# Performance work log

Measured on AMD Instinct MI355X. Metric: run time of the kernel, lower is better.

The kernel has to match this reference:

```python
import jax, jax.numpy as jnp
import numpy as np

N_NODES = 100000
N_EDGES = 3200000
D_IN, D_HID, D_OUT = 256, 256, 256
B, V, C = 64, 50, 64
DEC_H1, DEC_H2, N_CLS = 512, 256, 1000
NEG_INF = -1e9


def setup_inputs() -> dict:
    key = jax.random.key(0)
    ks = jax.random.split(key, 20)
    s = lambda d: 1.0 / np.sqrt(d)
    return {
        'edge_index': jax.random.randint(ks[0], (2, N_EDGES), 0, N_NODES, dtype=jnp.int64 if jax.config.jax_enable_x64 else jnp.int32),
        'edge_weight': jax.random.uniform(ks[1], (N_EDGES,), dtype=jnp.float32),
        'codes_x': jax.random.randint(ks[2], (B, V, C), 0, N_NODES, dtype=jnp.int64 if jax.config.jax_enable_x64 else jnp.int32),
        'node_emb': jax.random.normal(ks[3], (N_NODES, D_IN), jnp.float32) * 0.02,
        'W1': jax.random.normal(ks[4], (D_IN, D_HID), jnp.float32) * s(D_IN),
        'b1': jnp.zeros((D_HID,), jnp.float32),
        'W2': jax.random.normal(ks[5], (D_HID, D_OUT), jnp.float32) * s(D_HID),
        'b2': jnp.zeros((D_OUT,), jnp.float32),
        'Wv': jax.random.normal(ks[6], (D_OUT, D_OUT), jnp.float32) * s(D_OUT),
        'uv': jax.random.normal(ks[7], (D_OUT,), jnp.float32) * s(D_OUT),
        'Wp': jax.random.normal(ks[8], (D_OUT, D_OUT), jnp.float32) * s(D_OUT),
        'up': jax.random.normal(ks[9], (D_OUT,), jnp.float32) * s(D_OUT),
        'Wd1': jax.random.normal(ks[10], (D_OUT, DEC_H1), jnp.float32) * s(D_OUT),
        'bd1': jnp.zeros((DEC_H1,), jnp.float32),
        'Wd2': jax.random.normal(ks[11], (DEC_H1, DEC_H2), jnp.float32) * s(DEC_H1),
        'bd2': jnp.zeros((DEC_H2,), jnp.float32),
        'Wd3': jax.random.normal(ks[12], (DEC_H2, N_CLS), jnp.float32) * s(DEC_H2),
        'bd3': jnp.zeros((N_CLS,), jnp.float32),
    }


def reference(edge_index, edge_weight, codes_x, node_emb, W1, b1, W2, b2,
              Wv, uv, Wp, up, Wd1, bd1, Wd2, bd2, Wd3, bd3):
    n = node_emb.shape[0]
    src, dst = edge_index[0], edge_index[1]

    def agg(x):  # weighted message passing: out_i = sum_{e: dst=i} w_e * x[src_e]
        return jax.ops.segment_sum(x[src] * edge_weight[:, None], dst, num_segments=n)

    # 2-layer weighted GCN over the code ontology graph (dropout in eval mode)
    h = jax.nn.relu(agg(node_emb) @ W1 + b1)          # [N, D_hid]
    emb = agg(h) @ W2 + b2                             # [N, D_out]

    # Ragged per-visit code attention, vectorized with masks (code id 0 = padding)
    code_mask = codes_x > 0                            # [B, V, C]
    ce = emb[codes_x]                                  # [B, V, C, D]
    ev = jnp.tanh(jnp.einsum('bvcd,de->bvce', ce, Wv)) @ uv   # [B, V, C]
    av = jax.nn.softmax(jnp.where(code_mask, ev, NEG_INF), axis=-1)
    vemb = jnp.einsum('bvc,bvcd->bvd', av, ce)         # [B, V, D]
    visit_mask = code_mask.any(-1)                     # [B, V]
    vemb = jnp.where(visit_mask[..., None], vemb, 0.0)

    # Per-patient visit attention over valid visits only
    ep = jnp.tanh(vemb @ Wp) @ up                      # [B, V]
    ap = jax.nn.softmax(jnp.where(visit_mask, ep, NEG_INF), axis=-1)
    pemb = jnp.einsum('bv,bvd->bd', ap, vemb)          # [B, D]
    pemb = jnp.where(visit_mask.any(-1)[:, None], pemb, 0.0)  # empty patient -> zeros

    # Decoder MLP classifier (train_type='direct')
    h1 = jax.nn.relu(pemb @ Wd1 + bd1)
    h2 = jax.nn.relu(h1 @ Wd2 + bd2)
    return h2 @ Wd3 + bd3                              # [B, n_classes]
```

## Files before the change

### kernel.cpp

```cpp
#include <hip/hip_runtime.h>
#include <hip/hip_bf16.h>
#include <math.h>


#define D 256
#define BPAT 64
#define VIS 50
#define CODES 64
#define NEG_INF -1e9f
#define MPAD 100096
#define BINB 32
#define NBIN 3125
#define SORTCAP 1536

typedef unsigned short ushort_t;
typedef short short8 __attribute__((ext_vector_type(8)));
typedef float f32x4 __attribute__((ext_vector_type(4)));

__device__ __forceinline__ float blo(unsigned u) { return __uint_as_float(u << 16); }
__device__ __forceinline__ float bhi(unsigned u) { return __uint_as_float(u & 0xffff0000u); }
__device__ __forceinline__ float bf2f(ushort_t u) { return __uint_as_float((unsigned)u << 16); }
__device__ __forceinline__ ushort_t f2bfu(float f) {
    __hip_bfloat16 h = __float2bfloat16(f);
    return *reinterpret_cast<ushort_t*>(&h);
}
__device__ __forceinline__ unsigned pack2(float a, float b) {
    return (unsigned)f2bfu(a) | ((unsigned)f2bfu(b) << 16);
}
__device__ __forceinline__ float fast_tanh(float x) {
    return 1.f - 2.f / (__expf(2.f * x) + 1.f);
}

__global__ __launch_bounds__(512) void count_transpose_kernel(
    const int* __restrict__ ei, int* __restrict__ bincount, int ne,
    const float* __restrict__ Wa, const float* __restrict__ Wb,
    const float* __restrict__ Wc, const float* __restrict__ Wd,
    ushort_t* __restrict__ Ta, ushort_t* __restrict__ Tb,
    ushort_t* __restrict__ Tc, ushort_t* __restrict__ Td) {
    __shared__ int h[NBIN];
    __shared__ float tt[2][32][33];
    if (blockIdx.x < 256) {
        for (int i = threadIdx.x; i < NBIN; i += 512) h[i] = 0;
        __syncthreads();
        const int stride = 256 * 512;
        for (int e = blockIdx.x * 512 + threadIdx.x; e < ne; e += stride)
            atomicAdd(&h[ei[(size_t)ne + e] >> 5], 1);
        __syncthreads();
        for (int i = threadIdx.x; i < NBIN; i += 512) {
            int c = h[i];
            if (c) atomicAdd(&bincount[i], c);
        }
    } else {
        int tile = (blockIdx.x - 256) * 2 + (threadIdx.x >> 8);
        int which = tile >> 6, rem = tile & 63;
        int bx = (rem & 7) << 5, by = (rem >> 3) << 5;
        const float* W = (which == 0) ? Wa : (which == 1) ? Wb
                        : (which == 2) ? Wc : Wd;
        ushort_t* Wt = (which == 0) ? Ta : (which == 1) ? Tb
                      : (which == 2) ? Tc : Td;
        int hf = threadIdx.x >> 8;
        int ltid = threadIdx.x & 255;
        int lx = ltid & 31, ly = ltid >> 5;
        #pragma unroll
        for (int i = 0; i < 32; i += 8)
            tt[hf][ly + i][lx] = W[(size_t)(by + ly + i) * 256 + bx + lx];
        __syncthreads();
        #pragma unroll
        for (int i = 0; i < 32; i += 8)
            Wt[(size_t)(bx + ly + i) * 256 + by + lx] = f2bfu(tt[hf][lx][ly + i]);
    }
}

__global__ __launch_bounds__(64) void bin_scan_kernel(
    const int* __restrict__ bincount, int* __restrict__ binstart,
    int* __restrict__ bincursor, int* __restrict__ rp, int ne, int nn) {
    __shared__ int carry;
    int lane = threadIdx.x;
    if (lane == 0) carry = 0;
    __syncthreads();
    for (int base = 0; base < NBIN; base += 64) {
        int i = base + lane;
        int v = (i < NBIN) ? bincount[i] : 0;
        int x = v;
        #pragma unroll
        for (int d = 1; d < 64; d <<= 1) {
            int y = __shfl_up(x, (unsigned)d, 64);
            if (lane >= d) x += y;
        }
        int c = carry;
        if (i < NBIN) { int ex = c + x - v; binstart[i] = ex; bincursor[i] = ex; }
        __syncthreads();
        if (lane == 63) carry = c + x;
        __syncthreads();
    }
    if (lane == 0) { binstart[NBIN] = ne; rp[nn] = ne; }
}

__global__ __launch_bounds__(512) void part_gemm_kernel(
    const int* __restrict__ ei, const float* __restrict__ ew,
    int* __restrict__ bincursor, uint2* __restrict__ ptmp, int ne,
    const float* __restrict__ Af, const ushort_t* __restrict__ Wt,
    ushort_t* __restrict__ out, int nvalid) {
    __shared__ int h[NBIN];
    __shared__ int base_[NBIN];
    __shared__ __align__(16) ushort_t As[128 * 32];
    __shared__ __align__(16) ushort_t Bs[256 * 32];
    const int tid = threadIdx.x;
    if (blockIdx.x < 256) {
        for (int i = tid; i < NBIN; i += 512) h[i] = 0;
        __syncthreads();
        const int stride = 256 * 512;
        for (int e = blockIdx.x * 512 + tid; e < ne; e += stride)
            atomicAdd(&h[ei[(size_t)ne + e] >> 5], 1);
        __syncthreads();
        for (int i = tid; i < NBIN; i += 512) {
            int c = h[i];
            base_[i] = c ? atomicAdd(&bincursor[i], c) : 0;
            h[i] = 0;
        }
        __syncthreads();
        for (int e = blockIdx.x * 512 + tid; e < ne; e += stride) {
            int dd = ei[(size_t)ne + e];
            int ss = ei[e];
            float w = ew[e];
            int bin = dd >> 5;
            int r = atomicAdd(&h[bin], 1);
            ptmp[base_[bin] + r] =
                make_uint2((unsigned)ss | ((unsigned)(dd & 31) << 17),
                           __float_as_uint(w));
        }
        return;
    }
    const int gbid = blockIdx.x - 256;
    const int lane = tid & 63;
    const int wv = tid >> 6;
    const int wr = wv >> 2, wc = wv & 3;
    const size_t brow = (size_t)gbid * 128;

    const int ra = tid >> 2, ca = tid & 3;
    const int rb1 = ra + 128;
    const int csa = ca ^ ((ra >> 1) & 3);
    const int arow = (int)brow + ra;
    const bool aval = arow < nvalid;
    const float* gAf = Af + (size_t)arow * 256 + ca * 8;
    const ushort_t* gB0 = Wt + (size_t)ra  * 256 + ca * 8;
    const ushort_t* gB1 = Wt + (size_t)rb1 * 256 + ca * 8;
    ushort_t* lA  = As + ra * 32 + csa * 8;
    ushort_t* lB0 = Bs + ra * 32 + csa * 8;
    ushort_t* lB1 = Bs + rb1 * 32 + csa * 8;

    const int g = lane >> 4, rl = lane & 15;
    int aoff[4], boff[4];
    #pragma unroll
    for (int m = 0; m < 4; ++m) {
        int row = wr * 64 + m * 16 + rl;
        aoff[m] = row * 32 + (g ^ ((row >> 1) & 3)) * 8;
    }
    #pragma unroll
    for (int n = 0; n < 4; ++n) {
        int row = wc * 64 + n * 16 + rl;
        boff[n] = row * 32 + (g ^ ((row >> 1) & 3)) * 8;
    }

    f32x4 acc[4][4] = {};
    float4 pa0 = make_float4(0.f, 0.f, 0.f, 0.f), pa1 = pa0;
    if (aval) { pa0 = *(const float4*)gAf; pa1 = *(const float4*)(gAf + 4); }
    uint4 vb0 = *(const uint4*)gB0;
    uint4 vb1 = *(const uint4*)gB1;

    for (int ks = 0; ks < 8; ++ks) {
        uint4 va;
        va.x = pack2(pa0.x, pa0.y); va.y = pack2(pa0.z, pa0.w);
        va.z = pack2(pa1.x, pa1.y); va.w = pack2(pa1.z, pa1.w);
        *(uint4*)lA = va; *(uint4*)lB0 = vb0; *(uint4*)lB1 = vb1;
        __syncthreads();
        if (ks < 7) {
            int k0 = (ks + 1) * 32;
            if (aval) {
                pa0 = *(const float4*)(gAf + k0);
                pa1 = *(const float4*)(gAf + k0 + 4);
            }
            vb0 = *(const uint4*)(gB0 + k0);
            vb1 = *(const uint4*)(gB1 + k0);
        }
        short8 af[4], bfv[4];
        #pragma unroll
        for (int m = 0; m < 4; ++m) af[m] = *(const short8*)(As + aoff[m]);
        #pragma unroll
        for (int n = 0; n < 4; ++n) bfv[n] = *(const short8*)(Bs + boff[n]);
        #pragma unroll
        for (int m = 0; m < 4; ++m)
            #pragma unroll
            for (int n = 0; n < 4; ++n)
                acc[m][n] = __builtin_amdgcn_mfma_f32_16x16x32_bf16(
                    af[m], bfv[n], acc[m][n], 0, 0, 0);
        __syncthreads();
    }

    #pragma unroll
    for (int m = 0; m < 4; ++m) {
        #pragma unroll
        for (int r = 0; r < 4; ++r) {
            size_t row = brow + wr * 64 + m * 16 + g * 4 + r;
            #pragma unroll
            for (int n = 0; n < 4; ++n) {
                int col = wc * 64 + n * 16 + rl;
                out[row * 256 + col] = f2bfu(acc[m][n][r]);
            }
        }
    }
}

__global__ __launch_bounds__(256) void binsort_kernel(
    const uint2* __restrict__ ptmp, const int* __restrict__ binstart,
    uint2* __restrict__ epair, int* __restrict__ rp) {
    int b = blockIdx.x;
    int tid = threadIdx.x;
    int beg = binstart[b], end = binstart[b + 1];
    int nE = end - beg;
    __shared__ uint2 sbuf[SORTCAP];
    __shared__ int cnt[BINB];
    __shared__ int cur[BINB];
    if (tid < BINB) cnt[tid] = 0;
    __syncthreads();
    if (nE <= SORTCAP) {
        for (int i = tid; i < nE; i += 256) {
            uint2 p = ptmp[beg + i];
            sbuf[i] = p;
            atomicAdd(&cnt[(p.x >> 17) & 31], 1);
        }
        __syncthreads();
        if (tid < BINB) {
            int v = cnt[tid];
            int x = v;
            #pragma unroll
            for (int d = 1; d < BINB; d <<= 1) {
                int y = __shfl_up(x, (unsigned)d, BINB);
                if (tid >= d) x += y;
            }
            int start = beg + x - v;
            cur[tid] = start;
            rp[b * BINB + tid] = start;
        }
        __syncthreads();
        for (int i = tid; i < nE; i += 256) {
            uint2 p = sbuf[i];
            int dl = (p.x >> 17) & 31;
            int pos = atomicAdd(&cur[dl], 1);
            epair[pos] = make_uint2(p.x & 0x1FFFF, p.y);
        }
    } else {
        for (int i = beg + tid; i < end; i += 256)
            atomicAdd(&cnt[(ptmp[i].x >> 17) & 31], 1);
        __syncthreads();
        if (tid < BINB) {
            int v = cnt[tid];
            int x = v;
            #pragma unroll
            for (int d = 1; d < BINB; d <<= 1) {
                int y = __shfl_up(x, (unsigned)d, BINB);
                if (tid >= d) x += y;
            }
            int start = beg + x - v;
            cur[tid] = start;
            rp[b * BINB + tid] = start;
        }
        __syncthreads();
        for (int i = beg + tid; i < end; i += 256) {
            uint2 p = ptmp[i];
            int dl = (p.x >> 17) & 31;
            int pos = atomicAdd(&cur[dl], 1);
            epair[pos] = make_uint2(p.x & 0x1FFFF, p.y);
        }
    }
}

__device__ __forceinline__ void acc8(float* a, uint4 v, float w) {
    a[0] += w * blo(v.x); a[1] += w * bhi(v.x);
    a[2] += w * blo(v.y); a[3] += w * bhi(v.y);
    a[4] += w * blo(v.z); a[5] += w * bhi(v.z);
    a[6] += w * blo(v.w); a[7] += w * bhi(v.w);
}

template<int ACT>
__global__ __launch_bounds__(256) void agg_bf16_kernel(
    const ushort_t* __restrict__ x, const int* __restrict__ rp,
    const uint2* __restrict__ ep, const float* __restrict__ bias,
    ushort_t* __restrict__ out, int n) {
    int wv = (int)(((size_t)blockIdx.x * blockDim.x + threadIdx.x) >> 6);
    int lane = threadIdx.x & 63;
    if (wv >= n) return;
    int half = lane >> 5;
    int l32 = lane & 31;
    int beg = rp[wv], end = rp[wv + 1];
    float a[8] = {};
    int e = beg;
    for (; e + 16 <= end; e += 16) {
        uint2 p0 = ep[e + half];
        uint2 p1 = ep[e + 2 + half];
        uint2 p2 = ep[e + 4 + half];
        uint2 p3 = ep[e + 6 + half];
        uint2 p4 = ep[e + 8 + half];
        uint2 p5 = ep[e + 10 + half];
        uint2 p6 = ep[e + 12 + half];
        uint2 p7 = ep[e + 14 + half];
        uint4 v0 = ((const uint4*)(x + (size_t)p0.x * D))[l32];
        uint4 v1 = ((const uint4*)(x + (size_t)p1.x * D))[l32];
        uint4 v2 = ((const uint4*)(x + (size_t)p2.x * D))[l32];
        uint4 v3 = ((const uint4*)(x + (size_t)p3.x * D))[l32];
        uint4 v4 = ((const uint4*)(x + (size_t)p4.x * D))[l32];
        uint4 v5 = ((const uint4*)(x + (size_t)p5.x * D))[l32];
        uint4 v6 = ((const uint4*)(x + (size_t)p6.x * D))[l32];
        uint4 v7 = ((const uint4*)(x + (size_t)p7.x * D))[l32];
        acc8(a, v0, __uint_as_float(p0.y));
        acc8(a, v1, __uint_as_float(p1.y));
        acc8(a, v2, __uint_as_float(p2.y));
        acc8(a, v3, __uint_as_float(p3.y));
        acc8(a, v4, __uint_as_float(p4.y));
        acc8(a, v5, __uint_as_float(p5.y));
        acc8(a, v6, __uint_as_float(p6.y));
        acc8(a, v7, __uint_as_float(p7.y));
    }
    for (; e + 4 <= end; e += 4) {
        uint2 p0 = ep[e + half];
        uint2 p1 = ep[e + 2 + half];
        uint4 v0 = ((const uint4*)(x + (size_t)p0.x * D))[l32];
        uint4 v1 = ((const uint4*)(x + (size_t)p1.x * D))[l32];
        acc8(a, v0, __uint_as_float(p0.y));
        acc8(a, v1, __uint_as_float(p1.y));
    }
    for (; e + 2 <= end; e += 2) {
        uint2 p0 = ep[e + half];
        uint4 v0 = ((const uint4*)(x + (size_t)p0.x * D))[l32];
        acc8(a, v0, __uint_as_float(p0.y));
    }
    if (e < end) {
        uint2 p0 = ep[e];
        uint4 v0 = ((const uint4*)(x + (size_t)p0.x * D))[l32];
        acc8(a, v0, half ? 0.f : __uint_as_float(p0.y));
    }
    #pragma unroll
    for (int j = 0; j < 8; ++j) a[j] += __shfl_xor(a[j], 32, 64);
    if (half == 0) {
        float4 b0 = ((const float4*)bias)[l32 * 2];
        float4 b1 = ((const float4*)bias)[l32 * 2 + 1];
        a[0] += b0.x; a[1] += b0.y; a[2] += b0.z; a[3] += b0.w;
        a[4] += b1.x; a[5] += b1.y; a[6] += b1.z; a[7] += b1.w;
        if (ACT == 1) {
            #pragma unroll
            for (int j = 0; j < 8; ++j) a[j] = fmaxf(a[j], 0.f);
        }
        uint4 o;
        o.x = pack2(a[0], a[1]); o.y = pack2(a[2], a[3]);
        o.z = pack2(a[4], a[5]); o.w = pack2(a[6], a[7]);
        ((uint4*)(out + (size_t)wv * D))[l32] = o;
    }
}

template<int MODE>
__global__ __launch_bounds__(512) void mfma_gemm_kernel(
    const ushort_t* __restrict__ A, const ushort_t* __restrict__ Wt,
    const float* __restrict__ bias, ushort_t* __restrict__ out,
    const float* __restrict__ u, float* __restrict__ tout, int mvalid) {
    __shared__ __align__(16) ushort_t As[128 * 32];
    __shared__ __align__(16) ushort_t Bs[256 * 32];
    __shared__ float s_t[128];
    const int tid = threadIdx.x;
    const int lane = tid & 63;
    const int wv = tid >> 6;
    const int wr = wv >> 2, wc = wv & 3;
    const size_t brow = (size_t)blockIdx.x * 128;

    const int ra = tid >> 2, ca = tid & 3;
    const int rb1 = ra + 128;
    const int csa = ca ^ ((ra >> 1) & 3);
    const ushort_t* gA  = A  + (brow + ra) * 256 + ca * 8;
    const ushort_t* gB0 = Wt + (size_t)ra  * 256 + ca * 8;
    const ushort_t* gB1 = Wt + (size_t)rb1 * 256 + ca * 8;
    ushort_t* lA  = As + ra * 32 + csa * 8;
    ushort_t* lB0 = Bs + ra * 32 + csa * 8;
    ushort_t* lB1 = Bs + rb1 * 32 + csa * 8;

    const int g = lane >> 4, rl = lane & 15;
    int aoff[4], boff[4];
    #pragma unroll
    for (int m = 0; m < 4; ++m) {
        int row = wr * 64 + m * 16 + rl;
        aoff[m] = row * 32 + (g ^ ((row >> 1) & 3)) * 8;
    }
    #pragma unroll
    for (int n = 0; n < 4; ++n) {
        int row = wc * 64 + n * 16 + rl;
        boff[n] = row * 32 + (g ^ ((row >> 1) & 3)) * 8;
    }

    if (MODE == 2 && tid < 128) s_t[tid] = 0.f;

    f32x4 acc[4][4] = {};
    uint4 va  = *(const uint4*)gA;
    uint4 vb0 = *(const uint4*)gB0;
    uint4 vb1 = *(const uint4*)gB1;

    for (int ks = 0; ks < 8; ++ks) {
        *(uint4*)lA = va; *(uint4*)lB0 = vb0; *(uint4*)lB1 = vb1;
        __syncthreads();
        if (ks < 7) {
            int k0 = (ks + 1) * 32;
            va  = *(const uint4*)(gA + k0);
            vb0 = *(const uint4*)(gB0 + k0);
            vb1 = *(const uint4*)(gB1 + k0);
        }
        short8 af[4], bfv[4];
        #pragma unroll
        for (int m = 0; m < 4; ++m) af[m] = *(const short8*)(As + aoff[m]);
        #pragma unroll
        for (int n = 0; n < 4; ++n) bfv[n] = *(const short8*)(Bs + boff[n]);
        #pragma unroll
        for (int m = 0; m < 4; ++m)
            #pragma unroll
            for (int n = 0; n < 4; ++n)
                acc[m][n] = __builtin_amdgcn_mfma_f32_16x16x32_bf16(
                    af[m], bfv[n], acc[m][n], 0, 0, 0);
        __syncthreads();
    }

    if (MODE == 2) {
        float uvv[4];
        #pragma unroll
        for (int n = 0; n < 4; ++n) uvv[n] = u[wc * 64 + n * 16 + rl];
        #pragma unroll
        for (int m = 0; m < 4; ++m) {
            #pragma unroll
            for (int r = 0; r < 4; ++r) {
                float v = 0.f;
                #pragma unroll
                for (int n = 0; n < 4; ++n) v += fast_tanh(acc[m][n][r]) * uvv[n];
                v += __shfl_xor(v, 1, 64);
                v += __shfl_xor(v, 2, 64);
                v += __shfl_xor(v, 4, 64);
                v += __shfl_xor(v, 8, 64);
                if (rl == 0) atomicAdd(&s_t[wr * 64 + m * 16 + g * 4 + r], v);
            }
        }
        __syncthreads();
        if (tid < 128 && brow + tid < (size_t)mvalid) tout[brow + tid] = s_t[tid];
    } else {
        #pragma unroll
        for (int m = 0; m < 4; ++m) {
            #pragma unroll
            for (int r = 0; r < 4; ++r) {
                size_t row = brow + wr * 64 + m * 16 + g * 4 + r;
                #pragma unroll
                for (int n = 0; n < 4; ++n) {
                    int col = wc * 64 + n * 16 + rl;
                    float v = acc[m][n][r] + (bias ? bias[col] : 0.f);
                    out[row * 256 + col] = f2bfu(v);
                }
            }
        }
    }
}

__global__ __launch_bounds__(256) void code_attn_kernel(
    const int* __restrict__ codes, const float* __restrict__ t,
    const ushort_t* __restrict__ emb, ushort_t* __restrict__ vembB,
    int* __restrict__ vmask) {
    int bv = blockIdx.x;
    int tid = threadIdx.x;
    __shared__ int s_codes[CODES];
    __shared__ float s_av[CODES];
    __shared__ int s_valid;
    if (tid < 64) {
        int c = codes[(size_t)bv * CODES + tid];
        s_codes[tid] = c;
        float e = (c > 0) ? t[c] : NEG_INF;
        float m = e;
        #pragma unroll
        for (int d = 32; d; d >>= 1) m = fmaxf(m, __shfl_xor(m, d, 64));
        float ex = expf(e - m);
        float s = ex;
        #pragma unroll
        for (int d = 32; d; d >>= 1) s += __shfl_xor(s, d, 64);
        s_av[tid] = ex / s;
        if (tid == 0) s_valid = (m > -1e8f) ? 1 : 0;
    }
    __syncthreads();
    float acc = 0.f;
    #pragma unroll 8
    for (int c = 0; c < CODES; ++c)
        acc += s_av[c] * bf2f(emb[(size_t)s_codes[c] * D + tid]);
    int valid = s_valid;
    vembB[(size_t)bv * D + tid] = f2bfu(valid ? acc : 0.f);
    if (tid == 0) vmask[bv] = valid;
}

__global__ __launch_bounds__(512) void patient_dec_kernel(
    const ushort_t* __restrict__ vembB, const float* __restrict__ epr,
    const int* __restrict__ vmask,
    const float* __restrict__ Wd1, const float* __restrict__ bd1,
    const float* __restrict__ Wd2, const float* __restrict__ bd2,
    const float* __restrict__ Wd3, const float* __restrict__ bd3,
    float* __restrict__ outp) {
    int b = blockIdx.x;
    int tid = threadIdx.x;
    __shared__ float s_ap[VIS];
    __shared__ float s_x[256];
    __shared__ float s_h1[512];
    __shared__ float s_h2[256];
    __shared__ int s_any;

    if (tid < 64) {
        float e = -3e38f;
        if (tid < VIS) e = vmask[b * VIS + tid] ? epr[b * VIS + tid] : NEG_INF;
        float m = e;
        #pragma unroll
        for (int d = 32; d; d >>= 1) m = fmaxf(m, __shfl_xor(m, d, 64));
        float ex = (tid < VIS) ? expf(e - m) : 0.f;
        float s = ex;
        #pragma unroll
        for (int d = 32; d; d >>= 1) s += __shfl_xor(s, d, 64);
        if (tid < VIS) s_ap[tid] = ex / s;
        if (tid == 0) s_any = (m > -1e8f) ? 1 : 0;
    }
    __syncthreads();
    if (tid < 256) {
        float acc = 0.f;
        for (int v = 0; v < VIS; ++v)
            acc += s_ap[v] * bf2f(vembB[((size_t)b * VIS + v) * D + tid]);
        s_x[tid] = s_any ? acc : 0.f;
    }
    __syncthreads();
    {
        float acc = bd1[tid];
        #pragma unroll 8
        for (int k = 0; k < 256; ++k)
            acc = fmaf(s_x[k], Wd1[(size_t)k * 512 + tid], acc);
        s_h1[tid] = fmaxf(acc, 0.f);
    }
    __syncthreads();
    if (tid < 256) {
        float acc = bd2[tid];
        #pragma unroll 8
        for (int k = 0; k < 512; ++k)
            acc = fmaf(s_h1[k], Wd2[(size_t)k * 256 + tid], acc);
        s_h2[tid] = fmaxf(acc, 0.f);
    }
    __syncthreads();
    for (int j = tid; j < 1000; j += 512) {
        float acc = bd3[j];
        #pragma unroll 8
        for (int k = 0; k < 256; ++k)
            acc = fmaf(s_h2[k], Wd3[(size_t)k * 1000 + j], acc);
        outp[(size_t)b * 1000 + j] = acc;
    }
}

extern "C" void kernel_launch(void* const* d_in, const int* in_sizes, int n_in,
                              void* d_out, int out_size, void* d_ws, size_t ws_size,
                              hipStream_t stream) {
    const int* edge_index    = (const int*)d_in[0];
    const float* edge_weight = (const float*)d_in[1];
    const int* codes         = (const int*)d_in[2];
    const float* node_emb    = (const float*)d_in[3];
    const float* W1 = (const float*)d_in[4];
    const float* b1 = (const float*)d_in[5];
    const float* W2 = (const float*)d_in[6];
    const float* b2 = (const float*)d_in[7];
    const float* Wv = (const float*)d_in[8];
    const float* uv = (const float*)d_in[9];
    const float* Wp = (const float*)d_in[10];
    const float* up = (const float*)d_in[11];
    const float* Wd1 = (const float*)d_in[12];
    const float* bd1 = (const float*)d_in[13];
    const float* Wd2 = (const float*)d_in[14];
    const float* bd2 = (const float*)d_in[15];
    const float* Wd3 = (const float*)d_in[16];
    const float* bd3 = (const float*)d_in[17];

    const int NE = in_sizes[1];
    const int NN = in_sizes[3] / D;

    char* ws = (char*)d_ws;
    size_t off = 0;
    auto alloc = [&](size_t bytes) -> void* {
        void* p = ws + off;
        off += (bytes + 255) & ~(size_t)255;
        return p;
    };
    ushort_t* zbuf = (ushort_t*)alloc((size_t)MPAD * D * 2);
    ushort_t* hbuf = (ushort_t*)alloc((size_t)MPAD * D * 2);
    ushort_t* embB = (ushort_t*)alloc((size_t)MPAD * D * 2);
    uint2* ptmp   = (uint2*)alloc((size_t)NE * 8);
    uint2* epair  = (uint2*)alloc((size_t)NE * 8);
    int* bincount = (int*)alloc((size_t)NBIN * 4);
    int* binstart = (int*)alloc((size_t)(NBIN + 1) * 4);
    int* bincursor= (int*)alloc((size_t)NBIN * 4);
    int* rp       = (int*)alloc((size_t)(NN + 1) * 4);
    ushort_t* W1t = (ushort_t*)alloc(256 * 256 * 2);
    ushort_t* W2t = (ushort_t*)alloc(256 * 256 * 2);
    ushort_t* Wvt = (ushort_t*)alloc(256 * 256 * 2);
    ushort_t* Wpt = (ushort_t*)alloc(256 * 256 * 2);
    float* tbuf  = (float*)alloc((size_t)NN * 4);
    ushort_t* vembB = (ushort_t*)alloc((size_t)BPAT * VIS * D * 2);
    int*   vmask = (int*)  alloc((size_t)BPAT * VIS * 4);
    float* epr   = (float*)alloc((size_t)BPAT * VIS * 4);
    (void)ws_size; (void)n_in; (void)out_size;

    const int ab = NN / 4;

    hipMemsetAsync(bincount, 0, (size_t)NBIN * 4, stream);
    count_transpose_kernel<<<256 + 128, 512, 0, stream>>>(
        edge_index, bincount, NE, W1, W2, Wv, Wp, W1t, W2t, Wvt, Wpt);
    bin_scan_kernel<<<1, 64, 0, stream>>>(bincount, binstart, bincursor, rp, NE, NN);
    part_gemm_kernel<<<256 + MPAD / 128, 512, 0, stream>>>(
        edge_index, edge_weight, bincursor, ptmp, NE,
        node_emb, W1t, zbuf, NN);
    binsort_kernel<<<NBIN, 256, 0, stream>>>(ptmp, binstart, epair, rp);

    agg_bf16_kernel<1><<<ab, 256, 0, stream>>>(zbuf, rp, epair, b1, hbuf, NN);

    mfma_gemm_kernel<1><<<MPAD / 128, 512, 0, stream>>>(
        hbuf, W2t, nullptr, zbuf, nullptr, nullptr, 0);
    agg_bf16_kernel<0><<<ab, 256, 0, stream>>>(zbuf, rp, epair, b2, embB, NN);

    mfma_gemm_kernel<2><<<MPAD / 128, 512, 0, stream>>>(
        embB, Wvt, nullptr, nullptr, uv, tbuf, NN);

    code_attn_kernel<<<BPAT * VIS, 256, 0, stream>>>(codes, tbuf, embB, vembB, vmask);

    mfma_gemm_kernel<2><<<BPAT * VIS / 128, 512, 0, stream>>>(
        vembB, Wpt, nullptr, nullptr, up, epr, BPAT * VIS);

    patient_dec_kernel<<<BPAT, 512, 0, stream>>>(
        vembB, epr, vmask, Wd1, bd1, Wd2, bd2, Wd3, bd3, (float*)d_out);
}
```

Baseline: 794.6 us.

## Split edge aggregation into two feature-half passes to shrink gather working set

```diff
diff --git a/kernel.cpp b/kernel.cpp
--- a/kernel.cpp
+++ b/kernel.cpp
@@ -275,15 +275,13 @@
     }
 }
 
-__device__ __forceinline__ void acc8(float* a, uint4 v, float w) {
+__device__ __forceinline__ void acc4(float* a, uint2 v, float w) {
     a[0] += w * blo(v.x); a[1] += w * bhi(v.x);
     a[2] += w * blo(v.y); a[3] += w * bhi(v.y);
-    a[4] += w * blo(v.z); a[5] += w * bhi(v.z);
-    a[6] += w * blo(v.w); a[7] += w * bhi(v.w);
-}
-
-template<int ACT>
-__global__ __launch_bounds__(256) void agg_bf16_kernel(
+}
+
+template<int ACT, int PASS>
+__global__ __launch_bounds__(256) void agg_half_kernel(
     const ushort_t* __restrict__ x, const int* __restrict__ rp,
     const uint2* __restrict__ ep, const float* __restrict__ bias,
     ushort_t* __restrict__ out, int n) {
@@ -293,7 +291,8 @@
     int half = lane >> 5;
     int l32 = lane & 31;
     int beg = rp[wv], end = rp[wv + 1];
-    float a[8] = {};
+    const ushort_t* xh = x + PASS * 128;
+    float a[4] = {};
     int e = beg;
     for (; e + 16 <= end; e += 16) {
         uint2 p0 = ep[e + half];
@@ -304,56 +303,53 @@
         uint2 p5 = ep[e + 10 + half];
         uint2 p6 = ep[e + 12 + half];
         uint2 p7 = ep[e + 14 + half];
-        uint4 v0 = ((const uint4*)(x + (size_t)p0.x * D))[l32];
-        uint4 v1 = ((const uint4*)(x + (size_t)p1.x * D))[l32];
-        uint4 v2 = ((const uint4*)(x + (size_t)p2.x * D))[l32];
-        uint4 v3 = ((const uint4*)(x + (size_t)p3.x * D))[l32];
-        uint4 v4 = ((const uint4*)(x + (size_t)p4.x * D))[l32];
-        uint4 v5 = ((const uint4*)(x + (size_t)p5.x * D))[l32];
-        uint4 v6 = ((const uint4*)(x + (size_t)p6.x * D))[l32];
-        uint4 v7 = ((const uint4*)(x + (size_t)p7.x * D))[l32];
-        acc8(a, v0, __uint_as_float(p0.y));
-        acc8(a, v1, __uint_as_float(p1.y));
-        acc8(a, v2, __uint_as_float(p2.y));
-        acc8(a, v3, __uint_as_float(p3.y));
-        acc8(a, v4, __uint_as_float(p4.y));
-        acc8(a, v5, __uint_as_float(p5.y));
-        acc8(a, v6, __uint_as_float(p6.y));
-        acc8(a, v7, __uint_as_float(p7.y));
+        uint2 v0 = ((const uint2*)(xh + (size_t)p0.x * D))[l32];
+        uint2 v1 = ((const uint2*)(xh + (size_t)p1.x * D))[l32];
+        uint2 v2 = ((const uint2*)(xh + (size_t)p2.x * D))[l32];
+        uint2 v3 = ((const uint2*)(xh + (size_t)p3.x * D))[l32];
+        uint2 v4 = ((const uint2*)(xh + (size_t)p4.x * D))[l32];
+        uint2 v5 = ((const uint2*)(xh + (size_t)p5.x * D))[l32];
+        uint2 v6 = ((const uint2*)(xh + (size_t)p6.x * D))[l32];
+        uint2 v7 = ((const uint2*)(xh + (size_t)p7.x * D))[l32];
+        acc4(a, v0, __uint_as_float(p0.y));
+        acc4(a, v1, __uint_as_float(p1.y));
+        acc4(a, v2, __uint_as_float(p2.y));
+        acc4(a, v3, __uint_as_float(p3.y));
+        acc4(a, v4, __uint_as_float(p4.y));
+        acc4(a, v5, __uint_as_float(p5.y));
+        acc4(a, v6, __uint_as_float(p6.y));
+        acc4(a, v7, __uint_as_float(p7.y));
     }
     for (; e + 4 <= end; e += 4) {
         uint2 p0 = ep[e + half];
         uint2 p1 = ep[e + 2 + half];
-        uint4 v0 = ((const uint4*)(x + (size_t)p0.x * D))[l32];
-        uint4 v1 = ((const uint4*)(x + (size_t)p1.x * D))[l32];
-        acc8(a, v0, __uint_as_float(p0.y));
-        acc8(a, v1, __uint_as_float(p1.y));
+        uint2 v0 = ((const uint2*)(xh + (size_t)p0.x * D))[l32];
+        uint2 v1 = ((const uint2*)(xh + (size_t)p1.x * D))[l32];
+        acc4(a, v0, __uint_as_float(p0.y));
+        acc4(a, v1, __uint_as_float(p1.y));
     }
     for (; e + 2 <= end; e += 2) {
         uint2 p0 = ep[e + half];
-        uint4 v0 = ((const uint4*)(x + (size_t)p0.x * D))[l32];
-        acc8(a, v0, __uint_as_float(p0.y));
+        uint2 v0 = ((const uint2*)(xh + (size_t)p0.x * D))[l32];
+        acc4(a, v0, __uint_as_float(p0.y));
     }
     if (e < end) {
         uint2 p0 = ep[e];
-        uint4 v0 = ((const uint4*)(x + (size_t)p0.x * D))[l32];
-        acc8(a, v0, half ? 0.f : __uint_as_float(p0.y));
+        uint2 v0 = ((const uint2*)(xh + (size_t)p0.x * D))[l32];
+        acc4(a, v0, half ? 0.f : __uint_as_float(p0.y));
     }
     #pragma unroll
-    for (int j = 0; j < 8; ++j) a[j] += __shfl_xor(a[j], 32, 64);
+    for (int j = 0; j < 4; ++j) a[j] += __shfl_xor(a[j], 32, 64);
     if (half == 0) {
-        float4 b0 = ((const float4*)bias)[l32 * 2];
-        float4 b1 = ((const float4*)bias)[l32 * 2 + 1];
+        float4 b0 = ((const float4*)(bias + PASS * 128))[l32];
         a[0] += b0.x; a[1] += b0.y; a[2] += b0.z; a[3] += b0.w;
-        a[4] += b1.x; a[5] += b1.y; a[6] += b1.z; a[7] += b1.w;
         if (ACT == 1) {
             #pragma unroll
-            for (int j = 0; j < 8; ++j) a[j] = fmaxf(a[j], 0.f);
-        }
-        uint4 o;
+            for (int j = 0; j < 4; ++j) a[j] = fmaxf(a[j], 0.f);
+        }
+        uint2 o;
         o.x = pack2(a[0], a[1]); o.y = pack2(a[2], a[3]);
-        o.z = pack2(a[4], a[5]); o.w = pack2(a[6], a[7]);
-        ((uint4*)(out + (size_t)wv * D))[l32] = o;
+        ((uint2*)(out + (size_t)wv * D + PASS * 128))[l32] = o;
     }
 }
 
@@ -617,11 +613,13 @@
         node_emb, W1t, zbuf, NN);
     binsort_kernel<<<NBIN, 256, 0, stream>>>(ptmp, binstart, epair, rp);
 
-    agg_bf16_kernel<1><<<ab, 256, 0, stream>>>(zbuf, rp, epair, b1, hbuf, NN);
+    agg_half_kernel<1, 0><<<ab, 256, 0, stream>>>(zbuf, rp, epair, b1, hbuf, NN);
+    agg_half_kernel<1, 1><<<ab, 256, 0, stream>>>(zbuf, rp, epair, b1, hbuf, NN);
 
     mfma_gemm_kernel<1><<<MPAD / 128, 512, 0, stream>>>(
         hbuf, W2t, nullptr, zbuf, nullptr, nullptr, 0);
-    agg_bf16_kernel<0><<<ab, 256, 0, stream>>>(zbuf, rp, epair, b2, embB, NN);
+    agg_half_kernel<0, 0><<<ab, 256, 0, stream>>>(zbuf, rp, epair, b2, embB, NN);
+    agg_half_kernel<0, 1><<<ab, 256, 0, stream>>>(zbuf, rp, epair, b2, embB, NN);
 
     mfma_gemm_kernel<2><<<MPAD / 128, 512, 0, stream>>>(
         embB, Wvt, nullptr, nullptr, uv, tbuf, NN);
```

Measured after the change: 810.3 us. Within noise of the previous version (+2.0%).
